# Kernel tuning notes

Hardware: AMD Instinct MI355X
Metric: run time of the kernel (lower is better)

## Reference

```python
import jax, jax.numpy as jnp
import numpy as np

NUM = 8          # nlk*nlk - 1
IDX_REF = 4      # center neighbor index


def _gather2d(img, yi, xi):
    # img: (B,H,W); yi,xi: int32 (B,K,H,W) already clipped in-range
    B, H, W = img.shape
    flat = img.reshape(B, H * W)
    idx = (yi * W + xi).reshape(B, -1)
    return jnp.take_along_axis(flat, idx, axis=1).reshape(yi.shape)


def _bilinear(img, ys, xs):
    # bilinear sample with zero padding outside (deform-conv v2 semantics)
    # img: (B,H,W); ys,xs: float (B,K,H,W)
    B, H, W = img.shape
    y0 = jnp.floor(ys)
    x0 = jnp.floor(xs)
    y0i = y0.astype(jnp.int32)
    x0i = x0.astype(jnp.int32)
    wy1 = ys - y0
    wx1 = xs - x0
    out = jnp.zeros(ys.shape, img.dtype)
    for dy, wy in ((0, 1.0 - wy1), (1, wy1)):
        for dx, wx in ((0, 1.0 - wx1), (1, wx1)):
            yy = y0i + dy
            xx = x0i + dx
            valid = ((yy >= 0) & (yy < H) & (xx >= 0) & (xx < W)).astype(img.dtype)
            v = _gather2d(img, jnp.clip(yy, 0, H - 1), jnp.clip(xx, 0, W - 1))
            out = out + wy * wx * valid * v
    return out


def _conv3(x, w):
    return jax.lax.conv_general_dilated(x, w, (1, 1), ((1, 1), (1, 1)),
                                        dimension_numbers=('NCHW', 'OIHW', 'NCHW'))


def _bn_relu(x, g, b, m, v):
    s = g / jnp.sqrt(v + 1e-5)
    return jax.nn.relu(x * s[None, :, None, None] + (b - m * s)[None, :, None, None])


def _disp_warp(right, disp):
    # sample right image at x' = x - disparity, bilinear along width, zeros outside
    B, C, H, W = right.shape
    xs = jnp.arange(W, dtype=right.dtype)[None, None, :] - disp[:, 0]  # (B,H,W)
    x0 = jnp.floor(xs)
    x0i = x0.astype(jnp.int32)
    w1 = xs - x0
    out = jnp.zeros_like(right)
    for d, w in ((0, 1.0 - w1), (1, w1)):
        xi = x0i + d
        valid = ((xi >= 0) & (xi < W)).astype(right.dtype)
        v = jnp.take_along_axis(right, jnp.clip(xi, 0, W - 1)[:, None], axis=3)
        out = out + (w * valid)[:, None] * v
    return out


def _forward(coarse_disparity, normal_estimation, left_image, right_image, confidence,
             conv1_w, bn1_g, bn1_b, bn1_m, bn1_v,
             conv2_w, bn2_g, bn2_b, bn2_m, bn2_v,
             conv3_w, aff_scale_const):
    B, _, H, W = coarse_disparity.shape
    # current_scale == 1 => interpolate is identity, disp_ == coarse_disparity
    warped_error = _disp_warp(right_image, coarse_disparity) - left_image
    guidance = jnp.concatenate([normal_estimation, left_image, right_image, warped_error], axis=1)

    x = _bn_relu(_conv3(guidance, conv1_w), bn1_g, bn1_b, bn1_m, bn1_v)
    x = _bn_relu(_conv3(x, conv2_w), bn2_g, bn2_b, bn2_m, bn2_v)
    oa = _conv3(x, conv3_w)                                   # (B, 3*NUM, H, W)

    o1, o2, aff = oa[:, :NUM], oa[:, NUM:2 * NUM], oa[:, 2 * NUM:]
    # torch: cat((o1,o2),1).view(B,NUM,2,H,W) -> faithful pairing of channels
    off = jnp.concatenate([o1, o2], axis=1).reshape(B, NUM, 2, H, W)
    zero_c = jnp.zeros((B, 1, 2, H, W), off.dtype)
    off9 = jnp.concatenate([off[:, :IDX_REF], zero_c, off[:, IDX_REF:]], axis=1)  # (B,9,2,H,W)

    aff = jnp.tanh(aff) / (aff_scale_const + 1e-8)            # TGASS

    # confidence gather at p + offset_k (1x1 deform conv, w_conf=1), offsets detached
    ii = jnp.arange(H, dtype=off.dtype)[None, None, :, None]
    jj = jnp.arange(W, dtype=off.dtype)[None, None, None, :]
    off_nc = jax.lax.stop_gradient(
        jnp.concatenate([off9[:, :IDX_REF], off9[:, IDX_REF + 1:]], axis=1))  # (B,8,2,H,W)
    conf_aff = _bilinear(confidence[:, 0], ii + off_nc[:, :, 0], jj + off_nc[:, :, 1])
    aff = aff * conf_aff

    s = jnp.sum(jnp.abs(aff), axis=1, keepdims=True) + 1e-4
    s = jnp.maximum(s, 1.0)                                   # TGASS clamp
    aff = aff / s
    aff_ref = 1.0 - jnp.sum(aff, axis=1, keepdims=True)
    aff9 = jnp.concatenate([aff[:, :IDX_REF], aff_ref, aff[:, IDX_REF:]], axis=1)  # (B,9,H,W)

    # one propagation: modulated deformable 3x3 conv, all-ones weight, zero bias
    ky = (jnp.arange(9, dtype=off.dtype) // 3 - 1.0)[None, :, None, None]
    kx = (jnp.arange(9, dtype=off.dtype) % 3 - 1.0)[None, :, None, None]
    sampled = _bilinear(coarse_disparity[:, 0], ii + ky + off9[:, :, 0], jj + kx + off9[:, :, 1])
    inter = jnp.sum(aff9 * sampled, axis=1, keepdims=True)    # (B,1,H,W)
    inter = inter * (inter >= 0).astype(inter.dtype)
    inter = jnp.maximum(inter, 0.0)
    final = jnp.maximum(0.7 * coarse_disparity + 0.3 * inter, 0.0)
    return final


def setup_inputs() -> dict:
    key = jax.random.key(0)
    ks = jax.random.split(key, 20)
    B, H, W = 4, 384, 1280
    inp = {}
    inp['coarse_disparity'] = jax.random.uniform(ks[0], (B, 1, H, W), jnp.float32) * 40.0
    inp['normal_estimation'] = jax.random.normal(ks[1], (B, 3, H, W), jnp.float32)
    inp['left_image'] = jax.random.uniform(ks[2], (B, 3, H, W), jnp.float32)
    inp['right_image'] = jax.random.uniform(ks[3], (B, 3, H, W), jnp.float32)
    inp['confidence'] = jax.random.uniform(ks[4], (B, 1, H, W), jnp.float32)
    inp['conv1_w'] = jax.random.normal(ks[5], (32, 12, 3, 3), jnp.float32) * 0.05
    inp['bn1_g'] = jax.random.uniform(ks[6], (32,), jnp.float32) + 0.5
    inp['bn1_b'] = jax.random.normal(ks[7], (32,), jnp.float32) * 0.1
    inp['bn1_m'] = jax.random.normal(ks[8], (32,), jnp.float32) * 0.1
    inp['bn1_v'] = jax.random.uniform(ks[9], (32,), jnp.float32) + 0.5
    inp['conv2_w'] = jax.random.normal(ks[10], (64, 32, 3, 3), jnp.float32) * 0.05
    inp['bn2_g'] = jax.random.uniform(ks[11], (64,), jnp.float32) + 0.5
    inp['bn2_b'] = jax.random.normal(ks[12], (64,), jnp.float32) * 0.1
    inp['bn2_m'] = jax.random.normal(ks[13], (64,), jnp.float32) * 0.1
    inp['bn2_v'] = jax.random.uniform(ks[14], (64,), jnp.float32) + 0.5
    inp['conv3_w'] = jax.random.normal(ks[15], (3 * NUM, 64, 3, 3), jnp.float32) * 0.05
    inp['aff_scale_const'] = jnp.array([1.0 * NUM], jnp.float32)  # affinity_gamma * num
    return inp


def reference(coarse_disparity, normal_estimation, left_image, right_image, confidence,
              conv1_w, bn1_g, bn1_b, bn1_m, bn1_v,
              conv2_w, bn2_g, bn2_b, bn2_m, bn2_v,
              conv3_w, aff_scale_const):
    return _forward(coarse_disparity, normal_estimation, left_image, right_image, confidence,
                    conv1_w, bn1_g, bn1_b, bn1_m, bn1_v,
                    conv2_w, bn2_g, bn2_b, bn2_m, bn2_v,
                    conv3_w, aff_scale_const)
```

## Files before the change

### kernel.cpp

```cpp
#include <hip/hip_runtime.h>
#include <math.h>

static constexpr int B_ = 4;
static constexpr int H_ = 384;
static constexpr int W_ = 1280;
static constexpr int HW_ = H_ * W_;

typedef _Float16 f16x8 __attribute__((ext_vector_type(8)));
typedef float f32x4 __attribute__((ext_vector_type(4)));


__global__ __launch_bounds__(256) void guidance16(
    const float* __restrict__ disp, const float* __restrict__ normal,
    const float* __restrict__ left, const float* __restrict__ right,
    unsigned short* __restrict__ g16, int b0, int g, int y0g, int rows)
{
  int idx = blockIdx.x * 256 + threadIdx.x;
  if (idx >= g * rows * W_) return;
  int x = idx % W_;
  int t = idx / W_;
  int yr = t % rows;
  int gi = t / rows;
  int y = y0g + yr;
  int b = b0 + gi;
  int p = y * W_ + x;

  float d = disp[(size_t)b * HW_ + p];
  float xs = (float)x - d;
  float x0f = floorf(xs);
  int x0 = (int)x0f;
  float w1 = xs - x0f;
  int xi0 = x0, xi1 = x0 + 1;
  float v0 = (xi0 >= 0 && xi0 < W_) ? 1.f : 0.f;
  float v1 = (xi1 >= 0 && xi1 < W_) ? 1.f : 0.f;
  int xc0 = min(max(xi0, 0), W_ - 1);
  int xc1 = min(max(xi1, 0), W_ - 1);
  float w0f = (1.f - w1) * v0;
  float w1f = w1 * v1;

  union { _Float16 f[16]; uint4 u[2]; } R;
#pragma unroll
  for (int c = 0; c < 3; c++) {
    const float* rrow = right + (size_t)(b * 3 + c) * HW_ + (size_t)y * W_;
    float l = left[(size_t)(b * 3 + c) * HW_ + p];
    float n = normal[(size_t)(b * 3 + c) * HW_ + p];
    float r = rrow[x];
    float warped = w0f * rrow[xc0] + w1f * rrow[xc1];
    R.f[c]     = (_Float16)n;
    R.f[3 + c] = (_Float16)l;
    R.f[6 + c] = (_Float16)r;
    R.f[9 + c] = (_Float16)(warped - l);
  }
  R.f[12] = (_Float16)0.f; R.f[13] = (_Float16)0.f;
  R.f[14] = (_Float16)0.f; R.f[15] = (_Float16)0.f;

  unsigned short* dst = g16 + (((size_t)gi * rows + yr) * W_ + x) * 16;
  *(uint4*)(dst)     = R.u[0];
  *(uint4*)(dst + 8) = R.u[1];
}

template <int C_IN, int C_OUT>
__global__ __launch_bounds__(256) void prep_w(const float* __restrict__ w,
                                              unsigned short* __restrict__ wb)
{
  constexpr int CICH = C_IN / 32;
  constexpr int NCOT = (C_OUT + 15) / 16;
  constexpr int NE = NCOT * CICH * 9 * 512;
  int i = blockIdx.x * 256 + threadIdx.x;
  if (i >= NE) return;
  int k   = i & 31;
  int row = (i >> 5) & 15;
  int ts  = i >> 9;
  int s   = ts % 9;
  int tc  = ts / 9;
  int c   = tc % CICH;
  int t   = tc / CICH;
  int co  = t * 16 + row;
  int ci  = c * 32 + k;
  float v = 0.f;
  if (co < C_OUT) v = w[((size_t)co * C_IN + ci) * 9 + s];
  union { _Float16 f; unsigned short u; } ch;
  ch.f = (_Float16)v;
  wb[i] = ch.u;
}

__global__ __launch_bounds__(256) void prep_w1(const float* __restrict__ w,
                                               unsigned short* __restrict__ wb)
{
  constexpr int NE = 2 * 6 * 512;
  int i = blockIdx.x * 256 + threadIdx.x;
  if (i >= NE) return;
  int k    = i & 31;
  int row  = (i >> 5) & 15;
  int ts   = i >> 9;
  int chunk = ts % 6;
  int tc   = ts / 6;
  int ky   = chunk >> 1;
  int kc   = chunk & 1;
  int kx, ci;
  bool valid;
  if (kc == 0) { kx = k >> 4;  ci = k & 15; valid = (ci < 12); }
  else         { kx = 2;       ci = k & 15; valid = (k < 16) && (ci < 12); }
  int co = tc * 16 + row;
  float v = valid ? w[((size_t)co * 12 + ci) * 9 + ky * 3 + kx] : 0.f;
  union { _Float16 f; unsigned short u; } ch;
  ch.f = (_Float16)v;
  wb[i] = ch.u;
}

__global__ __launch_bounds__(256, 6) void conv1_mfma(
    const unsigned short* __restrict__ g16, const unsigned short* __restrict__ wb,
    const float* __restrict__ bn_g, const float* __restrict__ bn_b,
    const float* __restrict__ bn_m, const float* __restrict__ bn_v,
    unsigned short* __restrict__ out,
    int in_y0, int in_rows, int out_y0, int out_rows)
{
  constexpr int NCOT = 2;
  constexpr int TY  = 8;
  constexpr int HR  = 10;
  constexpr int TXI = 36;

  __shared__ unsigned short smem[HR * TXI * 16];

  const int tilesX = W_ / 32;
  int bb = blockIdx.x;
  const int txi = bb % tilesX; bb /= tilesX;
  const int tilesY = (out_rows + TY - 1) / TY;
  const int tyi = bb % tilesY;
  const int gi  = bb / tilesY;
  const int x0  = txi * 32;
  const int oy0 = out_y0 + tyi * TY;

  const int tid    = threadIdx.x;
  const int w      = tid >> 6;
  const int lane15 = tid & 15;
  const int kgrp   = (tid >> 4) & 3;
  const int aoff   = lane15 * 32 + kgrp * 8;

  f32x4 acc[NCOT][2][2];
#pragma unroll
  for (int i = 0; i < NCOT; i++)
#pragma unroll
    for (int rr = 0; rr < 2; rr++) {
      acc[i][rr][0] = (f32x4){0.f, 0.f, 0.f, 0.f};
      acc[i][rr][1] = (f32x4){0.f, 0.f, 0.f, 0.f};
    }

  for (int it = tid; it < HR * TXI; it += 256) {
    int row = it / TXI;
    int px  = it - row * TXI;
    int gy  = oy0 - 1 + row;
    int by  = gy - in_y0;
    int gx  = x0 - 2 + px;
    uint4 u0 = {0, 0, 0, 0}, u1 = {0, 0, 0, 0};
    if (((unsigned)by < (unsigned)in_rows) & ((unsigned)gx < (unsigned)W_)) {
      const unsigned short* src = g16 + (((size_t)gi * in_rows + by) * W_ + gx) * 16;
      u0 = *(const uint4*)(src);
      u1 = *(const uint4*)(src + 8);
    }
    unsigned short* dst = &smem[it * 16];
    *(uint4*)(dst)     = u0;
    *(uint4*)(dst + 8) = u1;
  }
  __syncthreads();

  f16x8 ah[NCOT];
#pragma unroll
  for (int tc = 0; tc < NCOT; tc++)
    ah[tc] = *(const f16x8*)(wb + ((size_t)(tc * 6 + 0) * 512 + aoff));
#pragma unroll
  for (int c = 0; c < 6; c++) {
    const int ky = c >> 1, kc = c & 1;
    f16x8 ahn[NCOT];
    if (c < 5) {
#pragma unroll
      for (int tc = 0; tc < NCOT; tc++)
        ahn[tc] = *(const f16x8*)(wb + ((size_t)(tc * 6 + c + 1) * 512 + aoff));
    }
#pragma unroll
    for (int rr = 0; rr < 2; rr++) {
      const int col = (kc ? 3 : 1) + lane15;
      const int e0 = ((2 * w + rr + ky) * TXI + col) * 16 + kgrp * 8;
      f16x8 b0 = *(const f16x8*)&smem[e0];
      f16x8 b1 = *(const f16x8*)&smem[e0 + 256];
#pragma unroll
      for (int tc = 0; tc < NCOT; tc++) {
        acc[tc][rr][0] = __builtin_amdgcn_mfma_f32_16x16x32_f16(
            ah[tc], b0, acc[tc][rr][0], 0, 0, 0);
        acc[tc][rr][1] = __builtin_amdgcn_mfma_f32_16x16x32_f16(
            ah[tc], b1, acc[tc][rr][1], 0, 0, 0);
      }
    }
    if (c < 5) {
#pragma unroll
      for (int tc = 0; tc < NCOT; tc++) ah[tc] = ahn[tc];
    }
  }

#pragma unroll
  for (int rr = 0; rr < 2; rr++) {
    const int orow = oy0 + 2 * w + rr;
    if (orow < out_y0 + out_rows) {
      const int ox = x0 + lane15;
#pragma unroll
      for (int tc = 0; tc < NCOT; tc++) {
        const int o = tc * 2 + (kgrp >> 1);
        const size_t recbase =
            (((size_t)(gi * 4 + o) * out_rows + (orow - out_y0)) * W_ + ox) * 8
            + (kgrp & 1) * 4;
#pragma unroll
        for (int nt = 0; nt < 2; nt++) {
          union { _Float16 f[4]; uint2 u; } Hh;
#pragma unroll
          for (int j = 0; j < 4; j++) {
            const int co = tc * 16 + kgrp * 4 + j;
            float s = bn_g[co] * rsqrtf(bn_v[co] + 1e-5f);
            float v = fmaxf(acc[tc][rr][nt][j] * s + (bn_b[co] - bn_m[co] * s), 0.f);
            Hh.f[j] = (_Float16)v;
          }
          *(uint2*)&out[recbase + (size_t)nt * 128] = Hh.u;
        }
      }
    }
  }
}

template <int C_IN, int C_OUT, bool BNRELU, bool OF16, int MINW>
__global__ __launch_bounds__(256, MINW) void conv3x3_mfma(
    const unsigned short* __restrict__ in, const unsigned short* __restrict__ wb,
    const float* __restrict__ bn_g, const float* __restrict__ bn_b,
    const float* __restrict__ bn_m, const float* __restrict__ bn_v,
    void* __restrict__ out,
    int in_y0, int in_rows, int out_y0, int out_rows)
{
  constexpr int CICH = C_IN / 32;
  constexpr int NCIO = C_IN / 8;
  constexpr int NCOT = (C_OUT + 15) / 16;
  constexpr int TY  = 8;
  constexpr int HR  = 10;
  constexpr int TXI = 36;
  constexpr int PX2 = 18;
  constexpr int PXW = 36;

  __shared__ unsigned short smem[HR * TXI * PXW];

  const int tilesX = W_ / 32;
  int bb = blockIdx.x;
  const int txi = bb % tilesX; bb /= tilesX;
  const int tilesY = (out_rows + TY - 1) / TY;
  const int tyi = bb % tilesY;
  const int gi  = bb / tilesY;
  const int x0  = txi * 32;
  const int oy0 = out_y0 + tyi * TY;

  const int tid    = threadIdx.x;
  const int w      = tid >> 6;
  const int lane15 = tid & 15;
  const int kgrp   = (tid >> 4) & 3;
  const int aoff   = lane15 * 32 + kgrp * 8;

  f32x4 acc[NCOT][2][2];
#pragma unroll
  for (int i = 0; i < NCOT; i++)
#pragma unroll
    for (int rr = 0; rr < 2; rr++) {
      acc[i][rr][0] = (f32x4){0.f, 0.f, 0.f, 0.f};
      acc[i][rr][1] = (f32x4){0.f, 0.f, 0.f, 0.f};
    }

  for (int cc = 0; cc < CICH; ++cc) {
    if (cc) __syncthreads();
    for (int it = tid; it < 4 * HR * PX2; it += 256) {
      int cib = it / (HR * PX2);
      int pos = it - cib * (HR * PX2);
      int row = pos / PX2;
      int p2  = pos - row * PX2;
      int gy  = oy0 - 1 + row;
      int by  = gy - in_y0;
      int gx  = x0 - 2 + 2 * p2;
      const bool rok = (unsigned)by < (unsigned)in_rows;
      uint4 h0 = {0,0,0,0}, h1 = {0,0,0,0};
      const unsigned short* src =
          in + (((size_t)(gi * NCIO + cc * 4 + cib) * in_rows + by) * W_ + gx) * 8;
      if (rok & ((unsigned)gx < (unsigned)W_))       h0 = *(const uint4*)(src);
      if (rok & ((unsigned)(gx + 1) < (unsigned)W_)) h1 = *(const uint4*)(src + 8);
      int base = (row * TXI + 2 * p2) * PXW + cib * 8;
      *(uint4*)&smem[base]       = h0;
      *(uint4*)&smem[base + PXW] = h1;
    }
    __syncthreads();

#pragma unroll
    for (int s = 0; s < 9; s++) {
      const int ky = s / 3, kx = s - 3 * ky;
      f16x8 ah[NCOT];
#pragma unroll
      for (int tc = 0; tc < NCOT; tc++)
        ah[tc] = *(const f16x8*)(
            wb + ((size_t)((tc * CICH + cc) * 9 + s) * 512 + aoff));
#pragma unroll
      for (int rr = 0; rr < 2; rr++) {
        const int e0 = ((2 * w + rr + ky) * TXI + 1 + lane15 + kx) * PXW + kgrp * 8;
        f16x8 b0 = *(const f16x8*)&smem[e0];
        f16x8 b1 = *(const f16x8*)&smem[e0 + 16 * PXW];
#pragma unroll
        for (int tc = 0; tc < NCOT; tc++) {
          acc[tc][rr][0] = __builtin_amdgcn_mfma_f32_16x16x32_f16(
              ah[tc], b0, acc[tc][rr][0], 0, 0, 0);
          acc[tc][rr][1] = __builtin_amdgcn_mfma_f32_16x16x32_f16(
              ah[tc], b1, acc[tc][rr][1], 0, 0, 0);
        }
      }
    }
  }

#pragma unroll
  for (int rr = 0; rr < 2; rr++) {
    const int orow = oy0 + 2 * w + rr;
    if (orow < out_y0 + out_rows) {
      const int ox = x0 + lane15;
      if constexpr (OF16) {
        unsigned short* outs = (unsigned short*)out;
#pragma unroll
        for (int tc = 0; tc < NCOT; tc++) {
          const int o = tc * 2 + (kgrp >> 1);
          const size_t recbase =
              (((size_t)(gi * (C_OUT / 8) + o) * out_rows + (orow - out_y0)) * W_ + ox) * 8
              + (kgrp & 1) * 4;
#pragma unroll
          for (int nt = 0; nt < 2; nt++) {
            union { _Float16 f[4]; uint2 u; } Hh;
#pragma unroll
            for (int j = 0; j < 4; j++) {
              float v = acc[tc][rr][nt][j];
              if constexpr (BNRELU) {
                const int co = tc * 16 + kgrp * 4 + j;
                float s = bn_g[co] * rsqrtf(bn_v[co] + 1e-5f);
                v = fmaxf(v * s + (bn_b[co] - bn_m[co] * s), 0.f);
              }
              Hh.f[j] = (_Float16)v;
            }
            *(uint2*)&outs[recbase + (size_t)nt * 128] = Hh.u;
          }
        }
      } else {
        float* outf = (float*)out;
#pragma unroll
        for (int tc = 0; tc < NCOT; tc++) {
#pragma unroll
          for (int j = 0; j < 4; j++) {
            const int co = tc * 16 + kgrp * 4 + j;
            if (co < C_OUT) {
              float r0 = acc[tc][rr][0][j];
              float r1 = acc[tc][rr][1][j];
              if constexpr (BNRELU) {
                float sc = bn_g[co] * rsqrtf(bn_v[co] + 1e-5f);
                float of = bn_b[co] - bn_m[co] * sc;
                r0 = fmaxf(r0 * sc + of, 0.f);
                r1 = fmaxf(r1 * sc + of, 0.f);
              }
              float* bp = outf + ((size_t)(gi * C_OUT + co) * out_rows +
                                  (orow - out_y0)) * (size_t)W_;
              bp[ox]      = r0;
              bp[ox + 16] = r1;
            }
          }
        }
      }
    }
  }
}

__device__ __forceinline__ float bilin1(const float* __restrict__ img,
                                        float ys, float xs)
{
  float y0f = floorf(ys), x0f = floorf(xs);
  int y0 = (int)y0f, x0 = (int)x0f;
  float wy1 = ys - y0f, wx1 = xs - x0f;
  float wy0 = 1.f - wy1, wx0 = 1.f - wx1;
  int y1 = y0 + 1, x1 = x0 + 1;
  float vy0 = (y0 >= 0 && y0 < H_) ? 1.f : 0.f;
  float vy1 = (y1 >= 0 && y1 < H_) ? 1.f : 0.f;
  float vx0 = (x0 >= 0 && x0 < W_) ? 1.f : 0.f;
  float vx1 = (x1 >= 0 && x1 < W_) ? 1.f : 0.f;
  int yc0 = min(max(y0, 0), H_ - 1), yc1 = min(max(y1, 0), H_ - 1);
  int xc0 = min(max(x0, 0), W_ - 1), xc1 = min(max(x1, 0), W_ - 1);
  const float* r0 = img + (size_t)yc0 * W_;
  const float* r1 = img + (size_t)yc1 * W_;
  float v00 = r0[xc0], v01 = r0[xc1], v10 = r1[xc0], v11 = r1[xc1];
  return (wy0 * vy0) * ((wx0 * vx0) * v00 + (wx1 * vx1) * v01) +
         (wy1 * vy1) * ((wx0 * vx0) * v10 + (wx1 * vx1) * v11);
}

__global__ __launch_bounds__(256) void final_band(
    const float* __restrict__ oa, const float* __restrict__ conf,
    const float* __restrict__ disp, const float* __restrict__ asc,
    float* __restrict__ out, int b0, int g, int y0g, int rows)
{
  int idx = blockIdx.x * 256 + threadIdx.x;
  if (idx >= g * rows * W_) return;
  int x = idx % W_;
  int t = idx / W_;
  int yr = t % rows;
  int gi = t / rows;
  int y = y0g + yr;
  int b = b0 + gi;
  int p = y * W_ + x;

  const float scale = 1.f / (asc[0] + 1e-8f);
  const float* cimg = conf + (size_t)b * HW_;
  const float* dimg = disp + (size_t)b * HW_;
  const float* oab = oa + (size_t)gi * 24 * rows * W_;
  const size_t cs = (size_t)rows * W_;
  const size_t q = (size_t)yr * W_ + x;

  float offy[8], offx[8], a[8];
#pragma unroll
  for (int k = 0; k < 8; k++) {
    offy[k] = oab[(size_t)k * cs + q];
    offx[k] = oab[(size_t)(8 + k) * cs + q];
    float ar = oab[(size_t)(16 + k) * cs + q];
    float ca = bilin1(cimg, (float)y + offy[k], (float)x + offx[k]);
    a[k] = tanhf(ar) * scale * ca;
  }

  float s = 1e-4f;
#pragma unroll
  for (int k = 0; k < 8; k++) s += fabsf(a[k]);
  s = fmaxf(s, 1.f);
  float inv = 1.f / s;
  float suma = 0.f;
#pragma unroll
  for (int k = 0; k < 8; k++) { a[k] *= inv; suma += a[k]; }
  float aref = 1.f - suma;

  float inter = 0.f;
#pragma unroll
  for (int k9 = 0; k9 < 9; k9++) {
    float oy, ox, w;
    if (k9 < 4)       { oy = offy[k9];     ox = offx[k9];     w = a[k9]; }
    else if (k9 == 4) { oy = 0.f;          ox = 0.f;          w = aref;  }
    else              { oy = offy[k9 - 1]; ox = offx[k9 - 1]; w = a[k9 - 1]; }
    float ky = (float)(k9 / 3) - 1.f;
    float kx = (float)(k9 % 3) - 1.f;
    inter += w * bilin1(dimg, (float)y + ky + oy, (float)x + kx + ox);
  }
  inter = fmaxf(inter, 0.f);
  float cd = dimg[p];
  out[(size_t)b * HW_ + p] = fmaxf(0.7f * cd + 0.3f * inter, 0.f);
}

extern "C" void kernel_launch(void* const* d_in, const int* in_sizes, int n_in,
                              void* d_out, int out_size, void* d_ws, size_t ws_size,
                              hipStream_t stream)
{
  const float* disp   = (const float*)d_in[0];
  const float* normal = (const float*)d_in[1];
  const float* left   = (const float*)d_in[2];
  const float* right  = (const float*)d_in[3];
  const float* conf   = (const float*)d_in[4];
  const float* w1     = (const float*)d_in[5];
  const float* g1     = (const float*)d_in[6];
  const float* b1     = (const float*)d_in[7];
  const float* m1     = (const float*)d_in[8];
  const float* v1     = (const float*)d_in[9];
  const float* w2     = (const float*)d_in[10];
  const float* g2     = (const float*)d_in[11];
  const float* b2     = (const float*)d_in[12];
  const float* m2     = (const float*)d_in[13];
  const float* v2     = (const float*)d_in[14];
  const float* w3     = (const float*)d_in[15];
  const float* asc    = (const float*)d_in[16];
  float* out = (float*)d_out;

  constexpr int WB1E = 2 * 6 * 512;
  constexpr int WB2E = 4 * 1 * 9 * 512;
  constexpr int WB3E = 2 * 2 * 9 * 512;
  const size_t wbytes = (size_t)(WB1E + WB2E + WB3E) * sizeof(unsigned short);

  struct Cfg { int g, bh; };
  const Cfg cfgs[] = {{4, 384}, {2, 384}, {1, 384}, {4, 96}, {2, 96},
                      {1, 96}, {1, 48}, {1, 24}, {1, 12}, {1, 8}, {1, 4}};
  int G = 1, BH = 4;
  for (const Cfg& c : cfgs) {
    size_t bytes = (size_t)c.g * W_ *
                   (32u * (c.bh + 6) + 64u * (c.bh + 4) + 128u * (c.bh + 2));
    if (bytes + wbytes <= ws_size) { G = c.g; BH = c.bh; break; }
  }

  unsigned short* g16 = (unsigned short*)d_ws;
  unsigned short* x1s = g16 + (size_t)G * (BH + 6) * W_ * 16;
  unsigned short* x2s = x1s + (size_t)G * 32 * (BH + 4) * W_;
  float* oa_buf = (float*)d_ws;
  unsigned short* wb1 = x2s + (size_t)G * 64 * (BH + 2) * W_;
  unsigned short* wb2 = wb1 + WB1E;
  unsigned short* wb3 = wb2 + WB2E;

  prep_w1<<<(WB1E + 255) / 256, 256, 0, stream>>>(w1, wb1);
  prep_w<32, 64><<<(WB2E + 255) / 256, 256, 0, stream>>>(w2, wb2);
  prep_w<64, 24><<<(WB3E + 255) / 256, 256, 0, stream>>>(w3, wb3);

  const int tilesX = W_ / 32;

  for (int b0 = 0; b0 < B_; b0 += G) {
    for (int y0 = 0; y0 < H_; y0 += BH) {
      const int rows_out = min(BH, H_ - y0);
      const int y_x2_0 = max(y0 - 1, 0);
      const int y_x2_1 = min(y0 + rows_out + 1, H_);
      const int rows_x2 = y_x2_1 - y_x2_0;
      const int y_x1_0 = max(y0 - 2, 0);
      const int y_x1_1 = min(y0 + rows_out + 2, H_);
      const int rows_x1 = y_x1_1 - y_x1_0;
      const int y_g_0 = max(y0 - 3, 0);
      const int y_g_1 = min(y0 + rows_out + 3, H_);
      const int rows_g = y_g_1 - y_g_0;

      {
        int n = G * rows_g * W_;
        guidance16<<<(n + 255) / 256, 256, 0, stream>>>(
            disp, normal, left, right, g16, b0, G, y_g_0, rows_g);
      }
      {
        int grid = tilesX * ((rows_x1 + 7) / 8) * G;
        conv1_mfma<<<grid, 256, 0, stream>>>(
            g16, wb1, g1, b1, m1, v1, x1s,
            y_g_0, rows_g, y_x1_0, rows_x1);
      }
      {
        int grid = tilesX * ((rows_x2 + 7) / 8) * G;
        conv3x3_mfma<32, 64, true, true, 4><<<grid, 256, 0, stream>>>(
            x1s, wb2, g2, b2, m2, v2, (void*)x2s,
            y_x1_0, rows_x1, y_x2_0, rows_x2);
      }
      {
        int grid = tilesX * ((rows_out + 7) / 8) * G;
        conv3x3_mfma<64, 24, false, false, 4><<<grid, 256, 0, stream>>>(
            x2s, wb3, nullptr, nullptr, nullptr, nullptr, (void*)oa_buf,
            y_x2_0, rows_x2, y0, rows_out);
      }
      {
        int n = G * rows_out * W_;
        final_band<<<(n + 255) / 256, 256, 0, stream>>>(
            oa_buf, conf, disp, asc, out, b0, G, y0, rows_out);
      }
    }
  }
}
```

Before: 593.3 us.

## Fuse guidance computation into conv1 and store conv3 offsets as fp16

The separate guidance kernel is removed, and conv1 now computes the disparity-warped guidance features straight from the fp32 inputs while it fills shared memory. This drops the write and re-read of the 16-channel fp16 guidance buffer and one kernel launch per band. Conv3 also gains an fp16 planar output mode that final_band reads, which halves offset and affinity traffic. The cost is recomputing guidance for the halo pixels, gathering the right image inside conv1, a lower occupancy bound on conv1, and reduced precision of offsets and affinities.

Measured after the change: 582.2 us. About the same (-1.9%).

```diff
diff --git a/kernel.cpp b/kernel.cpp
--- a/kernel.cpp
+++ b/kernel.cpp
@@ -9,55 +9,6 @@
 typedef _Float16 f16x8 __attribute__((ext_vector_type(8)));
 typedef float f32x4 __attribute__((ext_vector_type(4)));
 
-
-__global__ __launch_bounds__(256) void guidance16(
-    const float* __restrict__ disp, const float* __restrict__ normal,
-    const float* __restrict__ left, const float* __restrict__ right,
-    unsigned short* __restrict__ g16, int b0, int g, int y0g, int rows)
-{
-  int idx = blockIdx.x * 256 + threadIdx.x;
-  if (idx >= g * rows * W_) return;
-  int x = idx % W_;
-  int t = idx / W_;
-  int yr = t % rows;
-  int gi = t / rows;
-  int y = y0g + yr;
-  int b = b0 + gi;
-  int p = y * W_ + x;
-
-  float d = disp[(size_t)b * HW_ + p];
-  float xs = (float)x - d;
-  float x0f = floorf(xs);
-  int x0 = (int)x0f;
-  float w1 = xs - x0f;
-  int xi0 = x0, xi1 = x0 + 1;
-  float v0 = (xi0 >= 0 && xi0 < W_) ? 1.f : 0.f;
-  float v1 = (xi1 >= 0 && xi1 < W_) ? 1.f : 0.f;
-  int xc0 = min(max(xi0, 0), W_ - 1);
-  int xc1 = min(max(xi1, 0), W_ - 1);
-  float w0f = (1.f - w1) * v0;
-  float w1f = w1 * v1;
-
-  union { _Float16 f[16]; uint4 u[2]; } R;
-#pragma unroll
-  for (int c = 0; c < 3; c++) {
-    const float* rrow = right + (size_t)(b * 3 + c) * HW_ + (size_t)y * W_;
-    float l = left[(size_t)(b * 3 + c) * HW_ + p];
-    float n = normal[(size_t)(b * 3 + c) * HW_ + p];
-    float r = rrow[x];
-    float warped = w0f * rrow[xc0] + w1f * rrow[xc1];
-    R.f[c]     = (_Float16)n;
-    R.f[3 + c] = (_Float16)l;
-    R.f[6 + c] = (_Float16)r;
-    R.f[9 + c] = (_Float16)(warped - l);
-  }
-  R.f[12] = (_Float16)0.f; R.f[13] = (_Float16)0.f;
-  R.f[14] = (_Float16)0.f; R.f[15] = (_Float16)0.f;
-
-  unsigned short* dst = g16 + (((size_t)gi * rows + yr) * W_ + x) * 16;
-  *(uint4*)(dst)     = R.u[0];
-  *(uint4*)(dst + 8) = R.u[1];
-}
 
 template <int C_IN, int C_OUT>
 __global__ __launch_bounds__(256) void prep_w(const float* __restrict__ w,
@@ -108,12 +59,14 @@
   wb[i] = ch.u;
 }
 
-__global__ __launch_bounds__(256, 6) void conv1_mfma(
-    const unsigned short* __restrict__ g16, const unsigned short* __restrict__ wb,
+__global__ __launch_bounds__(256, 4) void conv1_mfma(
+    const float* __restrict__ disp, const float* __restrict__ normal,
+    const float* __restrict__ left, const float* __restrict__ right,
+    const unsigned short* __restrict__ wb,
     const float* __restrict__ bn_g, const float* __restrict__ bn_b,
     const float* __restrict__ bn_m, const float* __restrict__ bn_v,
     unsigned short* __restrict__ out,
-    int in_y0, int in_rows, int out_y0, int out_rows)
+    int b0, int out_y0, int out_rows)
 {
   constexpr int NCOT = 2;
   constexpr int TY  = 8;
@@ -128,6 +81,7 @@
   const int tilesY = (out_rows + TY - 1) / TY;
   const int tyi = bb % tilesY;
   const int gi  = bb / tilesY;
+  const int b   = b0 + gi;
   const int x0  = txi * 32;
   const int oy0 = out_y0 + tyi * TY;
 
@@ -150,17 +104,40 @@
     int row = it / TXI;
     int px  = it - row * TXI;
     int gy  = oy0 - 1 + row;
-    int by  = gy - in_y0;
     int gx  = x0 - 2 + px;
-    uint4 u0 = {0, 0, 0, 0}, u1 = {0, 0, 0, 0};
-    if (((unsigned)by < (unsigned)in_rows) & ((unsigned)gx < (unsigned)W_)) {
-      const unsigned short* src = g16 + (((size_t)gi * in_rows + by) * W_ + gx) * 16;
-      u0 = *(const uint4*)(src);
-      u1 = *(const uint4*)(src + 8);
+    union { _Float16 f[16]; uint4 u[2]; } R;
+    R.u[0] = (uint4){0, 0, 0, 0};
+    R.u[1] = (uint4){0, 0, 0, 0};
+    if (((unsigned)gy < (unsigned)H_) & ((unsigned)gx < (unsigned)W_)) {
+      size_t p = (size_t)gy * W_ + gx;
+      float d = disp[(size_t)b * HW_ + p];
+      float xs = (float)gx - d;
+      float x0f = floorf(xs);
+      int xi0 = (int)x0f;
+      float w1 = xs - x0f;
+      int xi1 = xi0 + 1;
+      float v0 = (xi0 >= 0 && xi0 < W_) ? 1.f : 0.f;
+      float v1 = (xi1 >= 0 && xi1 < W_) ? 1.f : 0.f;
+      int xc0 = min(max(xi0, 0), W_ - 1);
+      int xc1 = min(max(xi1, 0), W_ - 1);
+      float w0f = (1.f - w1) * v0;
+      float w1f = w1 * v1;
+#pragma unroll
+      for (int c = 0; c < 3; c++) {
+        const float* rrow = right + (size_t)(b * 3 + c) * HW_ + (size_t)gy * W_;
+        float l = left[(size_t)(b * 3 + c) * HW_ + p];
+        float n = normal[(size_t)(b * 3 + c) * HW_ + p];
+        float r = rrow[gx];
+        float warped = w0f * rrow[xc0] + w1f * rrow[xc1];
+        R.f[c]     = (_Float16)n;
+        R.f[3 + c] = (_Float16)l;
+        R.f[6 + c] = (_Float16)r;
+        R.f[9 + c] = (_Float16)(warped - l);
+      }
     }
     unsigned short* dst = &smem[it * 16];
-    *(uint4*)(dst)     = u0;
-    *(uint4*)(dst + 8) = u1;
+    *(uint4*)(dst)     = R.u[0];
+    *(uint4*)(dst + 8) = R.u[1];
   }
   __syncthreads();
 
@@ -225,7 +202,7 @@
   }
 }
 
-template <int C_IN, int C_OUT, bool BNRELU, bool OF16, int MINW>
+template <int C_IN, int C_OUT, bool BNRELU, int OUTMODE, int MINW>
 __global__ __launch_bounds__(256, MINW) void conv3x3_mfma(
     const unsigned short* __restrict__ in, const unsigned short* __restrict__ wb,
     const float* __restrict__ bn_g, const float* __restrict__ bn_b,
@@ -319,7 +296,7 @@
     const int orow = oy0 + 2 * w + rr;
     if (orow < out_y0 + out_rows) {
       const int ox = x0 + lane15;
-      if constexpr (OF16) {
+      if constexpr (OUTMODE == 1) {
         unsigned short* outs = (unsigned short*)out;
 #pragma unroll
         for (int tc = 0; tc < NCOT; tc++) {
@@ -341,6 +318,31 @@
               Hh.f[j] = (_Float16)v;
             }
             *(uint2*)&outs[recbase + (size_t)nt * 128] = Hh.u;
+          }
+        }
+      } else if constexpr (OUTMODE == 2) {
+        unsigned short* outs = (unsigned short*)out;
+#pragma unroll
+        for (int tc = 0; tc < NCOT; tc++) {
+#pragma unroll
+          for (int j = 0; j < 4; j++) {
+            const int co = tc * 16 + kgrp * 4 + j;
+            if (co < C_OUT) {
+              float r0 = acc[tc][rr][0][j];
+              float r1 = acc[tc][rr][1][j];
+              if constexpr (BNRELU) {
+                float sc = bn_g[co] * rsqrtf(bn_v[co] + 1e-5f);
+                float of = bn_b[co] - bn_m[co] * sc;
+                r0 = fmaxf(r0 * sc + of, 0.f);
+                r1 = fmaxf(r1 * sc + of, 0.f);
+              }
+              unsigned short* bp = outs + ((size_t)(gi * C_OUT + co) * out_rows +
+                                           (orow - out_y0)) * (size_t)W_;
+              union { _Float16 f; unsigned short u; } c0, c1;
+              c0.f = (_Float16)r0; c1.f = (_Float16)r1;
+              bp[ox]      = c0.u;
+              bp[ox + 16] = c1.u;
+            }
           }
         }
       } else {
@@ -393,7 +395,7 @@
 }
 
 __global__ __launch_bounds__(256) void final_band(
-    const float* __restrict__ oa, const float* __restrict__ conf,
+    const unsigned short* __restrict__ oa, const float* __restrict__ conf,
     const float* __restrict__ disp, const float* __restrict__ asc,
     float* __restrict__ out, int b0, int g, int y0g, int rows)
 {
@@ -410,16 +412,16 @@
   const float scale = 1.f / (asc[0] + 1e-8f);
   const float* cimg = conf + (size_t)b * HW_;
   const float* dimg = disp + (size_t)b * HW_;
-  const float* oab = oa + (size_t)gi * 24 * rows * W_;
+  const unsigned short* oab = oa + (size_t)gi * 24 * rows * W_;
   const size_t cs = (size_t)rows * W_;
   const size_t q = (size_t)yr * W_ + x;
 
   float offy[8], offx[8], a[8];
 #pragma unroll
   for (int k = 0; k < 8; k++) {
-    offy[k] = oab[(size_t)k * cs + q];
-    offx[k] = oab[(size_t)(8 + k) * cs + q];
-    float ar = oab[(size_t)(16 + k) * cs + q];
+    offy[k] = (float)(*(const _Float16*)&oab[(size_t)k * cs + q]);
+    offx[k] = (float)(*(const _Float16*)&oab[(size_t)(8 + k) * cs + q]);
+    float ar = (float)(*(const _Float16*)&oab[(size_t)(16 + k) * cs + q]);
     float ca = bilin1(cimg, (float)y + offy[k], (float)x + offx[k]);
     a[k] = tanhf(ar) * scale * ca;
   }
@@ -484,14 +486,13 @@
   int G = 1, BH = 4;
   for (const Cfg& c : cfgs) {
     size_t bytes = (size_t)c.g * W_ *
-                   (32u * (c.bh + 6) + 64u * (c.bh + 4) + 128u * (c.bh + 2));
+                   (64u * (c.bh + 4) + 128u * (c.bh + 2));
     if (bytes + wbytes <= ws_size) { G = c.g; BH = c.bh; break; }
   }
 
-  unsigned short* g16 = (unsigned short*)d_ws;
-  unsigned short* x1s = g16 + (size_t)G * (BH + 6) * W_ * 16;
+  unsigned short* x1s = (unsigned short*)d_ws;
   unsigned short* x2s = x1s + (size_t)G * 32 * (BH + 4) * W_;
-  float* oa_buf = (float*)d_ws;
+  unsigned short* oa_buf = (unsigned short*)d_ws;
   unsigned short* wb1 = x2s + (size_t)G * 64 * (BH + 2) * W_;
   unsigned short* wb2 = wb1 + WB1E;
   unsigned short* wb3 = wb2 + WB2E;
@@ -511,30 +512,22 @@
       const int y_x1_0 = max(y0 - 2, 0);
       const int y_x1_1 = min(y0 + rows_out + 2, H_);
       const int rows_x1 = y_x1_1 - y_x1_0;
-      const int y_g_0 = max(y0 - 3, 0);
-      const int y_g_1 = min(y0 + rows_out + 3, H_);
-      const int rows_g = y_g_1 - y_g_0;
-
-      {
-        int n = G * rows_g * W_;
-        guidance16<<<(n + 255) / 256, 256, 0, stream>>>(
-            disp, normal, left, right, g16, b0, G, y_g_0, rows_g);
-      }
+
       {
         int grid = tilesX * ((rows_x1 + 7) / 8) * G;
         conv1_mfma<<<grid, 256, 0, stream>>>(
-            g16, wb1, g1, b1, m1, v1, x1s,
-            y_g_0, rows_g, y_x1_0, rows_x1);
+            disp, normal, left, right, wb1, g1, b1, m1, v1, x1s,
+            b0, y_x1_0, rows_x1);
       }
       {
         int grid = tilesX * ((rows_x2 + 7) / 8) * G;
-        conv3x3_mfma<32, 64, true, true, 4><<<grid, 256, 0, stream>>>(
+        conv3x3_mfma<32, 64, true, 1, 4><<<grid, 256, 0, stream>>>(
             x1s, wb2, g2, b2, m2, v2, (void*)x2s,
             y_x1_0, rows_x1, y_x2_0, rows_x2);
       }
       {
         int grid = tilesX * ((rows_out + 7) / 8) * G;
-        conv3x3_mfma<64, 24, false, false, 4><<<grid, 256, 0, stream>>>(
+        conv3x3_mfma<64, 24, false, 2, 4><<<grid, 256, 0, stream>>>(
             x2s, wb3, nullptr, nullptr, nullptr, nullptr, (void*)oa_buf,
             y_x2_0, rows_x2, y0, rows_out);
       }
```
